# Kernel tuning notes

Hardware: AMD Instinct MI355X
Metric: run time of the kernel (lower is better)

The kernel has to match this reference:

```python
import jax, jax.numpy as jnp
import numpy as np

B, N, DIM = 8, 512, 768
H, DH = 12, 64
INNER = H * DH
MLP = 3072
DEPTH = 4
EPS = 1e-5
LS = 0.1  # LayerScale init_eps for depth <= 18


def _ln(x, scale):
    # flax LayerNorm(use_bias=False): (x-mean)/sqrt(var+eps) * scale
    mu = jnp.mean(x, axis=-1, keepdims=True)
    var = jnp.mean(jnp.square(x - mu), axis=-1, keepdims=True)
    return (x - mu) * jax.lax.rsqrt(var + EPS) * scale


def setup_inputs() -> dict:
    key = jax.random.key(0)
    ks = jax.random.split(key, 13)
    s = 0.02
    inp = {
        "x": jax.random.normal(ks[0], (B, N, DIM), jnp.float32),
        "ln1": jnp.ones((DEPTH, DIM), jnp.float32),
        "Wq": jax.random.normal(ks[1], (DEPTH, DIM, INNER), jnp.float32) * s,
        "Wkv": jax.random.normal(ks[2], (DEPTH, DIM, 2 * INNER), jnp.float32) * s,
        "mix_pre": jax.random.normal(ks[3], (DEPTH, H, H), jnp.float32) * 0.1,
        "mix_post": jax.random.normal(ks[4], (DEPTH, H, H), jnp.float32) * 0.1,
        "Wo": jax.random.normal(ks[5], (DEPTH, INNER, DIM), jnp.float32) * s,
        "bo": jnp.zeros((DEPTH, DIM), jnp.float32),
        "ln2": jnp.ones((DEPTH, DIM), jnp.float32),
        "W1": jax.random.normal(ks[6], (DEPTH, DIM, MLP), jnp.float32) * s,
        "b1": jnp.zeros((DEPTH, MLP), jnp.float32),
        "W2": jax.random.normal(ks[7], (DEPTH, MLP, DIM), jnp.float32) * s,
        "b2": jnp.zeros((DEPTH, DIM), jnp.float32),
    }
    return inp


def _block(x, p):
    ln1, Wq, Wkv, mp, mq, Wo, bo, ln2, W1, b1, W2, b2 = p
    scale = DH ** -0.5
    h = _ln(x, ln1)
    q = h @ Wq                                  # [b,n,inner]
    kv = h @ Wkv
    k, v = jnp.split(kv, 2, axis=-1)
    def to_heads(t):
        return t.reshape(B, N, H, DH).transpose(0, 2, 1, 3)  # b h n d
    q, k, v = to_heads(q), to_heads(k), to_heads(v)
    dots = jnp.einsum('bhid,bhjd->bhij', q, k) * scale
    dots = jnp.einsum('bhij,hg->bgij', dots, mp)   # talking-heads pre-softmax
    attn = jax.nn.softmax(dots, axis=-1)
    attn = jnp.einsum('bhij,hg->bgij', attn, mq)   # talking-heads post-softmax
    o = jnp.einsum('bhij,bhjd->bhid', attn, v)
    o = o.transpose(0, 2, 1, 3).reshape(B, N, INNER)
    x = (o @ Wo + bo) * LS + x
    h2 = _ln(x, ln2)
    x = ((jax.nn.gelu(h2 @ W1 + b1) @ W2) + b2) * LS + x
    return x, None


def reference(x, ln1, Wq, Wkv, mix_pre, mix_post, Wo, bo, ln2, W1, b1, W2, b2):
    params = (ln1, Wq, Wkv, mix_pre, mix_post, Wo, bo, ln2, W1, b1, W2, b2)
    out, _ = jax.lax.scan(_block, x, params)
    return out
```

## Files before the change

### kernel.cpp

```cpp
#include <hip/hip_runtime.h>


#define LSCALE 0.1f

typedef __bf16 bf16;
typedef __bf16 bf16x8 __attribute__((ext_vector_type(8)));
typedef __bf16 bf16x4 __attribute__((ext_vector_type(4)));
typedef unsigned short ushort4v __attribute__((ext_vector_type(4)));
typedef float  f32x4  __attribute__((ext_vector_type(4)));

__device__ __forceinline__ void g2l16(const void* g, void* l) {
    __builtin_amdgcn_global_load_lds(
        (const __attribute__((address_space(1))) void*)g,
        (__attribute__((address_space(3))) void*)l, 16, 0, 0);
}

template<int EPI, bool PLANA = false>
__global__ __launch_bounds__(256, 2)
void gemm_bt(const bf16* __restrict__ A, int lda, long saz1, long saz2,
             const bf16* __restrict__ Bt, int ldb, long sbz1, long sbz2,
             void* __restrict__ Cv, int ldc, long scz1, long scz2,
             int M, int N, int K, int zmod,
             const float* __restrict__ bias, float scale)
{
    __shared__ __align__(16) char smem[35840];
    bf16* As = (bf16*)smem;
    bf16* Bs = (bf16*)(smem + 16384);
    bf16* Cs = (bf16*)smem;

    const int z  = blockIdx.z;
    const int z1 = z / zmod, z2 = z - z1 * zmod;
    const bf16* Ab = A  + saz1 * (long)z1 + saz2 * (long)z2;
    const bf16* Bb = Bt + sbz1 * (long)z1 + sbz2 * (long)z2;

    const int m0 = blockIdx.x * 128, n0 = blockIdx.y * 128;
    const int tid = threadIdx.x, w = tid >> 6, l = tid & 63;
    const int wr = (w >> 1) * 64, wc = (w & 1) * 64;
    const int lr = l & 15, lq = l >> 4;
    const int srow = l >> 2, scol8 = (l & 3) * 8;

    long abase = 0;
    if constexpr (PLANA)
        abase = (long)(m0 >> 9) * 393216 + (long)((m0 & 511) + w * 32) * 64;

    f32x4 acc[4][4];
#pragma unroll
    for (int i = 0; i < 4; i++)
#pragma unroll
        for (int j = 0; j < 4; j++)
#pragma unroll
            for (int r = 0; r < 4; r++) acc[i][j][r] = 0.f;

    for (int k0 = 0; k0 < K; k0 += 64) {
        const bf16* Ag;
        int ldaa;
        if constexpr (PLANA) {
            Ag = Ab + abase + ((long)(k0 >> 6)) * 32768;
            ldaa = 64;
        } else {
            Ag = Ab + (long)(m0 + w * 32) * lda + k0;
            ldaa = lda;
        }
        const bf16* Bg = Bb + (long)(n0 + w * 32) * ldb + k0;
        g2l16(Ag + (long)srow * ldaa + scol8,             As + w * 1024);
        g2l16(Ag + (long)(srow + 16) * ldaa + scol8,      As + w * 1024 + 512);
        g2l16(Ag + (long)srow * ldaa + 32 + scol8,        As + 4096 + w * 1024);
        g2l16(Ag + (long)(srow + 16) * ldaa + 32 + scol8, As + 4096 + w * 1024 + 512);
        g2l16(Bg + (long)srow * ldb + scol8,             Bs + w * 1024);
        g2l16(Bg + (long)(srow + 16) * ldb + scol8,      Bs + w * 1024 + 512);
        g2l16(Bg + (long)srow * ldb + 32 + scol8,        Bs + 4096 + w * 1024);
        g2l16(Bg + (long)(srow + 16) * ldb + 32 + scol8, Bs + 4096 + w * 1024 + 512);
        __syncthreads();

#pragma unroll
        for (int hh = 0; hh < 2; hh++) {
            bf16x8 fa[4], fb[4];
#pragma unroll
            for (int i = 0; i < 4; i++)
                fa[i] = *(const bf16x8*)(As + hh * 4096 + (wr + i * 16 + lr) * 32 + lq * 8);
#pragma unroll
            for (int i = 0; i < 4; i++)
                fb[i] = *(const bf16x8*)(Bs + hh * 4096 + (wc + i * 16 + lr) * 32 + lq * 8);
#pragma unroll
            for (int mi = 0; mi < 4; mi++)
#pragma unroll
                for (int ni = 0; ni < 4; ni++)
                    acc[mi][ni] = __builtin_amdgcn_mfma_f32_16x16x32_bf16(
                        fa[mi], fb[ni], acc[mi][ni], 0, 0, 0);
        }
        __syncthreads();
    }

#pragma unroll
    for (int ni = 0; ni < 4; ni++) {
        const int col = wc + ni * 16 + lr;
        float bv = 0.f;
        if (EPI == 1) bv = bias[n0 + col];
#pragma unroll
        for (int mi = 0; mi < 4; mi++) {
#pragma unroll
            for (int r = 0; r < 4; r++) {
                const int row = wr + mi * 16 + lq * 4 + r;
                float v = acc[mi][ni][r];
                if (EPI == 0) {
                    v *= scale;
                } else if (EPI == 1) {
                    const float xx = v + bv;
                    const float u  = 0.7978845608f * (xx + 0.044715f * xx * xx * xx);
                    const float th = 1.f - 2.f / (__expf(2.f * u) + 1.f);
                    v = 0.5f * xx * (1.f + th);
                }
                Cs[row * 136 + col] = (bf16)v;
            }
        }
    }
    __syncthreads();

    const long cb = scz1 * (long)z1 + scz2 * (long)z2;
    const int rrow = tid >> 4, cg = tid & 15;
#pragma unroll
    for (int p = 0; p < 8; p++) {
        const int row = p * 16 + rrow;
        const bf16x8 v = *(const bf16x8*)(Cs + row * 136 + cg * 8);
        *(bf16x8*)((bf16*)Cv + cb + (long)(m0 + row) * ldc + n0 + cg * 8) = v;
    }
}

template<int PLANO>
__global__ __launch_bounds__(256, 4)
void gemm_av(const bf16* __restrict__ S, const bf16* __restrict__ qkvc,
             bf16* __restrict__ oc)
{
    __shared__ __align__(16) char av_smem[9728];
    bf16* As  = (bf16*)av_smem;
    bf16* Bst = (bf16*)(av_smem + 4096);
    bf16* Cs  = (bf16*)av_smem;

    const int z = blockIdx.y, b = z / 12, g = z - b * 12;
    const bf16* Ab;
    int sld;
    if constexpr (PLANO) {
        Ab = S + (long)b * 3145728 + g * 512;
        sld = 6144;
    } else {
        Ab = S + (long)z * 262144;
        sld = 512;
    }
    const bf16* Bb = qkvc + (long)b * 1179648 + 1536 + g * 64;

    const int i0 = blockIdx.x * 64;
    const int tid = threadIdx.x, w = tid >> 6, l = tid & 63;
    const int lr = l & 15, lq = l >> 4;
    const int srow = l >> 2, scol8 = (l & 3) * 8;
    const int kp = tid >> 4, dq = tid & 15;
    const int kcol = ((((kp >> 2) ^ ((dq >> 1) & 3)) << 3) | ((kp & 3) << 1));

    f32x4 acc[4];
#pragma unroll
    for (int j = 0; j < 4; j++)
#pragma unroll
        for (int r = 0; r < 4; r++) acc[j][r] = 0.f;

    unsigned short* Bw = (unsigned short*)Bst;

    for (int k0 = 0; k0 < 512; k0 += 32) {
        const bf16* Ag = Ab + (long)(i0 + w * 16) * sld + k0;
        g2l16(Ag + (long)srow * sld + scol8, As + w * 512);

        const bf16* Bg = Bb + (long)(k0 + 2 * kp) * 2304 + dq * 4;
        ushort4v u0 = *(const ushort4v*)(Bg);
        ushort4v u1 = *(const ushort4v*)(Bg + 2304);
#pragma unroll
        for (int r = 0; r < 4; r++) {
            unsigned p = (unsigned)u0[r] | ((unsigned)u1[r] << 16);
            *(unsigned*)(Bw + (dq * 4 + r) * 40 + kcol) = p;
        }
        __syncthreads();

        bf16x8 fa = *(const bf16x8*)(As + (w * 16 + lr) * 32 + lq * 8);
        bf16x8 fb[4];
#pragma unroll
        for (int i = 0; i < 4; i++) {
            const int d = i * 16 + lr;
            fb[i] = *(const bf16x8*)(Bst + d * 40 + ((lq ^ ((d >> 3) & 3)) << 3));
        }
#pragma unroll
        for (int ni = 0; ni < 4; ni++)
            acc[ni] = __builtin_amdgcn_mfma_f32_16x16x32_bf16(
                fa, fb[ni], acc[ni], 0, 0, 0);
        __syncthreads();
    }

    if constexpr (PLANO) {
#pragma unroll
        for (int ni = 0; ni < 4; ni++)
#pragma unroll
            for (int r = 0; r < 4; r++)
                Cs[(w * 16 + lq * 4 + r) * 68 + ni * 16 + lr] = (bf16)acc[ni][r];
        __syncthreads();
        const int rr = tid >> 2, c16 = (tid & 3) * 16;
        bf16* orow = oc + ((long)z * 512 + i0 + rr) * 64 + c16;
        *(bf16x8*)(orow)     = *(const bf16x8*)(Cs + rr * 68 + c16);
        *(bf16x8*)(orow + 8) = *(const bf16x8*)(Cs + rr * 68 + c16 + 8);
    } else {
        bf16* Cb = oc + (long)b * 1179648 + g * 64;
#pragma unroll
        for (int ni = 0; ni < 4; ni++) {
            const int gc = ni * 16 + lr;
#pragma unroll
            for (int r = 0; r < 4; r++) {
                const int gr = i0 + w * 16 + lq * 4 + r;
                Cb[(long)gr * 2304 + gc] = (bf16)acc[ni][r];
            }
        }
    }
}

__global__ __launch_bounds__(256)
void tconv_k(const float* __restrict__ in, bf16* __restrict__ out,
             int K, int N)
{
    __shared__ float t[32][33];
    const int n0 = blockIdx.x * 32, k0 = blockIdx.y * 32;
    const int x = threadIdx.x, y = threadIdx.y;
#pragma unroll
    for (int yy = 0; yy < 4; yy++)
        t[y + yy * 8][x] = in[(long)(k0 + y + yy * 8) * N + n0 + x];
    __syncthreads();
#pragma unroll
    for (int yy = 0; yy < 4; yy++)
        out[(long)(n0 + y + yy * 8) * K + k0 + x] = (bf16)t[x][y + yy * 8];
}

__global__ __launch_bounds__(256)
void pre_k(const float* __restrict__ Wq, const float* __restrict__ Wkv,
           const float* __restrict__ Wo, const float* __restrict__ W1,
           const float* __restrict__ W2, bf16* __restrict__ WtAll,
           const float* __restrict__ x, float* __restrict__ xf,
           const float* __restrict__ gam, bf16* __restrict__ hout)
{
    __shared__ __align__(16) char pmem[16640];
    const int bxg = blockIdx.x;
    const int t = threadIdx.x;
    if (bxg < 6912) {
        float (*st)[65] = (float(*)[65])pmem;
        const int L = bxg / 1728;
        int bx = bxg - L * 1728;
        bf16* WtL = WtAll + (long)L * 7077888;
        const float* src; bf16* dst; int K, N, ntn;
        if (bx < 144) {
            src = Wq + (long)L * 589824;   dst = WtL;            K = 768;  N = 768;  ntn = 12;
        } else if (bx < 432) {
            bx -= 144;
            src = Wkv + (long)L * 1179648; dst = WtL + 589824;   K = 768;  N = 1536; ntn = 24;
        } else if (bx < 576) {
            bx -= 432;
            src = Wo + (long)L * 589824;   dst = WtL + 1769472;  K = 768;  N = 768;  ntn = 12;
        } else if (bx < 1152) {
            bx -= 576;
            src = W1 + (long)L * 2359296;  dst = WtL + 2359296;  K = 768;  N = 3072; ntn = 48;
        } else {
            bx -= 1152;
            src = W2 + (long)L * 2359296;  dst = WtL + 4718592;  K = 3072; N = 768;  ntn = 12;
        }
        const int n0 = (bx % ntn) * 64, k0 = (bx / ntn) * 64;
        const int r = t >> 4, c4 = (t & 15) * 4;
#pragma unroll
        for (int rr = 0; rr < 4; rr++) {
            const f32x4 v = *(const f32x4*)(src + (long)(k0 + r + rr * 16) * N + n0 + c4);
            st[r + rr * 16][c4 + 0] = v[0];
            st[r + rr * 16][c4 + 1] = v[1];
            st[r + rr * 16][c4 + 2] = v[2];
            st[r + rr * 16][c4 + 3] = v[3];
        }
        __syncthreads();
        const int kc = (t & 7) * 8;
#pragma unroll
        for (int p = 0; p < 2; p++) {
            const int n = p * 32 + (t >> 3);
            bf16x8 o;
#pragma unroll
            for (int e = 0; e < 8; e++) o[e] = (bf16)st[kc + e][n];
            *(bf16x8*)(dst + (long)(n0 + n) * K + k0 + kc) = o;
        }
    } else {
        const int row = bxg - 6912;
        float* ps  = (float*)pmem;
        float* pss = (float*)pmem + 4;
        const float* xin = x + (long)row * 768;
        float* xr = xf + (long)row * 768;
        float v[3];
#pragma unroll
        for (int i = 0; i < 3; i++) {
            const int c = t + i * 256;
            const float xv = xin[c];
            xr[c] = xv;
            v[i] = xv;
        }
        float s  = v[0] + v[1] + v[2];
        float ss = v[0] * v[0] + v[1] * v[1] + v[2] * v[2];
#pragma unroll
        for (int off = 32; off; off >>= 1) {
            s  += __shfl_xor(s, off);
            ss += __shfl_xor(ss, off);
        }
        const int wv = t >> 6, l = t & 63;
        if (l == 0) { ps[wv] = s; pss[wv] = ss; }
        __syncthreads();
        s  = ps[0] + ps[1] + ps[2] + ps[3];
        ss = pss[0] + pss[1] + pss[2] + pss[3];
        const float mu = s * (1.f / 768.f);
        const float rs = rsqrtf(ss * (1.f / 768.f) - mu * mu + 1e-5f);
        bf16* orow = hout + (long)row * 768;
#pragma unroll
        for (int i = 0; i < 3; i++) {
            const int c = t + i * 256;
            orow[c] = (bf16)((v[i] - mu) * rs * gam[c]);
        }
    }
}

__global__ __launch_bounds__(256)
void lnres_k(float* __restrict__ xf, const bf16* __restrict__ P0,
             const bf16* __restrict__ P1, const float* __restrict__ bias,
             const float* __restrict__ gam, bf16* __restrict__ out,
             const float* __restrict__ src)
{
    const int row = blockIdx.x, t = threadIdx.x;
    float* xr = xf + (long)row * 768;
    float v[3];
#pragma unroll
    for (int i = 0; i < 3; i++) {
        const int c = t + i * 256;
        float xv;
        if (src) {
            xv = src[(long)row * 768 + c];
            xr[c] = xv;
        } else if (P0) {
            xv = xr[c] + LSCALE * ((float)P0[(long)row * 768 + c] +
                                   (float)P1[(long)row * 768 + c] + bias[c]);
            xr[c] = xv;
        } else {
            xv = xr[c];
        }
        v[i] = xv;
    }
    float s  = v[0] + v[1] + v[2];
    float ss = v[0] * v[0] + v[1] * v[1] + v[2] * v[2];
#pragma unroll
    for (int off = 32; off; off >>= 1) {
        s  += __shfl_xor(s, off);
        ss += __shfl_xor(ss, off);
    }
    __shared__ float ps[4], pss[4];
    const int wv = t >> 6, l = t & 63;
    if (l == 0) { ps[wv] = s; pss[wv] = ss; }
    __syncthreads();
    s  = ps[0] + ps[1] + ps[2] + ps[3];
    ss = pss[0] + pss[1] + pss[2] + pss[3];
    const float mu = s * (1.f / 768.f);
    const float rs = rsqrtf(ss * (1.f / 768.f) - mu * mu + 1e-5f);
    bf16* orow = out + (long)row * 768;
#pragma unroll
    for (int i = 0; i < 3; i++) {
        const int c = t + i * 256;
        orow[c] = (bf16)((v[i] - mu) * rs * gam[c]);
    }
}

__global__ __launch_bounds__(256)
void outres_k(const float* __restrict__ xf, const bf16* __restrict__ P0,
              const bf16* __restrict__ P1, const float* __restrict__ bias,
              float* __restrict__ out)
{
    const long i4 = ((long)blockIdx.x * 256 + threadIdx.x) * 4;
    const int c = (int)(i4 % 768);
    const f32x4 xv = *(const f32x4*)(xf + i4);
    const bf16x4 p0 = *(const bf16x4*)(P0 + i4);
    const bf16x4 p1 = *(const bf16x4*)(P1 + i4);
    const f32x4 bv = *(const f32x4*)(bias + c);
    f32x4 o;
#pragma unroll
    for (int e = 0; e < 4; e++)
        o[e] = xv[e] + LSCALE * ((float)p0[e] + (float)p1[e] + bv[e]);
    *(f32x4*)(out + i4) = o;
}

template<int CONTIG>
__global__ __launch_bounds__(256)
void mixsm_k(bf16* __restrict__ S, const float* __restrict__ mp,
             const float* __restrict__ mq)
{
    __shared__ float buf[12][512];
    __shared__ float rds[12];
    const int b = blockIdx.y, i = blockIdx.x, t = threadIdx.x;
    const long pstr = CONTIG ? 512 : 262144;
    bf16* Sb = CONTIG ? S + ((long)b * 512 + i) * 6144
                      : S + ((long)b * 12 * 512 + i) * 512;

    float s0[12], s1[12];
#pragma unroll
    for (int h = 0; h < 12; h++) {
        union { unsigned u; bf16 v[2]; } p;
        p.u = *(const unsigned*)(Sb + h * pstr + 2 * t);
        s0[h] = (float)p.v[0];
        s1[h] = (float)p.v[1];
    }
#pragma unroll
    for (int g = 0; g < 12; g++) {
        float a0 = 0.f, a1 = 0.f;
#pragma unroll
        for (int h = 0; h < 12; h++) {
            const float m = mp[h * 12 + g];
            a0 += s0[h] * m;
            a1 += s1[h] * m;
        }
        *(float2*)(&buf[g][2 * t]) = make_float2(a0, a1);
    }
    __syncthreads();

    const int wv = t >> 6, l = t & 63;
    for (int g = wv; g < 12; g += 4) {
        float mx = -3.0e38f;
#pragma unroll
        for (int k = 0; k < 8; k++) mx = fmaxf(mx, buf[g][l + 64 * k]);
#pragma unroll
        for (int off = 32; off; off >>= 1) mx = fmaxf(mx, __shfl_xor(mx, off));
        float sm = 0.f;
#pragma unroll
        for (int k = 0; k < 8; k++) {
            const float e = __expf(buf[g][l + 64 * k] - mx);
            buf[g][l + 64 * k] = e;
            sm += e;
        }
#pragma unroll
        for (int off = 32; off; off >>= 1) sm += __shfl_xor(sm, off);
        if (l == 0) rds[g] = 1.f / sm;
    }
    __syncthreads();

    float e0[12], e1[12];
#pragma unroll
    for (int h = 0; h < 12; h++) {
        const float2 ee = *(const float2*)(&buf[h][2 * t]);
        const float rd = rds[h];
        e0[h] = ee.x * rd;
        e1[h] = ee.y * rd;
    }
#pragma unroll
    for (int g = 0; g < 12; g++) {
        float a0 = 0.f, a1 = 0.f;
#pragma unroll
        for (int h = 0; h < 12; h++) {
            const float m = mq[h * 12 + g];
            a0 += e0[h] * m;
            a1 += e1[h] * m;
        }
        union { unsigned u; bf16 v[2]; } p;
        p.v[0] = (bf16)a0;
        p.v[1] = (bf16)a1;
        *(unsigned*)(Sb + g * pstr + 2 * t) = p.u;
    }
}

extern "C" void kernel_launch(void* const* d_in, const int* in_sizes, int n_in,
                              void* d_out, int out_size, void* d_ws, size_t ws_size,
                              hipStream_t stream)
{
    (void)in_sizes; (void)n_in; (void)out_size;
    const float* x   = (const float*)d_in[0];
    const float* ln1 = (const float*)d_in[1];
    const float* Wq  = (const float*)d_in[2];
    const float* Wkv = (const float*)d_in[3];
    const float* mp  = (const float*)d_in[4];
    const float* mq  = (const float*)d_in[5];
    const float* Wo  = (const float*)d_in[6];
    const float* bo  = (const float*)d_in[7];
    const float* ln2 = (const float*)d_in[8];
    const float* W1  = (const float*)d_in[9];
    const float* b1  = (const float*)d_in[10];
    const float* W2  = (const float*)d_in[11];
    const float* b2  = (const float*)d_in[12];

    char* ws = (char*)d_ws;
    float* xf  = (float*)(ws);
    bf16* h    = (bf16*)(ws + 12582912);
    bf16* qkv  = (bf16*)(ws + 18874368);
    bf16* S    = (bf16*)(ws + 37748736);
    bf16* mid  = S;
    bf16* P0   = h;
    bf16* P1w2 = qkv;
    bf16* P1wo = S;
    const long P1W2_OFF = 3145728;
    const long P1WO_OFF = 12582912;

    const dim3 tb(32, 8);

    if (ws_size >= 150994944ull) {
        bf16* WtAll = (bf16*)(ws + 88080384);
        bf16* oP    = (bf16*)(ws + 144703488);

        pre_k<<<11008, 256, 0, stream>>>(Wq, Wkv, Wo, W1, W2, WtAll,
                                         x, xf, ln1, h);

        for (int L = 0; L < 4; L++) {
            bf16* WtL = WtAll + (long)L * 7077888;

            if (L > 0)
                lnres_k<<<4096, 256, 0, stream>>>(xf, P0, P1w2, b2 + (L - 1) * 768,
                                                  ln1 + L * 768, h, nullptr);

            gemm_bt<0><<<dim3(32, 18, 1), 256, 0, stream>>>(
                h, 768, 0, 0, WtL, 768, 0, 0,
                qkv, 2304, 0, 0, 4096, 2304, 768, 1, nullptr, 1.f);

            gemm_bt<0><<<dim3(4, 4, 96), 256, 0, stream>>>(
                qkv,       2304, 1179648, 64,
                qkv + 768, 2304, 1179648, 64,
                S,         6144, 3145728, 512,
                512, 512, 64, 12, nullptr, 0.125f);

            mixsm_k<1><<<dim3(512, 8), 256, 0, stream>>>(S, mp + L * 144, mq + L * 144);

            gemm_av<1><<<dim3(8, 96), 256, 0, stream>>>(S, qkv, oP);

            gemm_bt<4, true><<<dim3(32, 6, 2), 256, 0, stream>>>(
                oP, 64, 0, 196608, WtL + 1769472, 768, 0, 384,
                P0, 768, 0, P1WO_OFF, 4096, 768, 384, 2, nullptr, 1.f);

            lnres_k<<<4096, 256, 0, stream>>>(xf, P0, P1wo, bo + L * 768,
                                              ln2 + L * 768, h, nullptr);

            gemm_bt<1><<<dim3(32, 24, 1), 256, 0, stream>>>(
                h, 768, 0, 0, WtL + 2359296, 768, 0, 0,
                mid, 3072, 0, 0, 4096, 3072, 768, 1, b1 + L * 3072, 1.f);

            gemm_bt<4><<<dim3(32, 6, 2), 256, 0, stream>>>(
                mid, 3072, 0, 1536, WtL + 4718592, 3072, 0, 1536,
                P0, 768, 0, P1W2_OFF, 4096, 768, 1536, 2, nullptr, 1.f);
        }
    } else {
        bf16* Wt = (bf16*)(ws + 62914560);

        for (int L = 0; L < 4; L++) {
            tconv_k<<<dim3(24, 24), tb, 0, stream>>>(Wq + (long)L * 589824, Wt, 768, 768);
            tconv_k<<<dim3(48, 24), tb, 0, stream>>>(Wkv + (long)L * 1179648, Wt + 589824, 768, 1536);

            if (L == 0)
                lnres_k<<<4096, 256, 0, stream>>>(xf, nullptr, nullptr, nullptr,
                                                  ln1 + L * 768, h, x);
            else
                lnres_k<<<4096, 256, 0, stream>>>(xf, P0, P1w2, b2 + (L - 1) * 768,
                                                  ln1 + L * 768, h, nullptr);

            gemm_bt<0><<<dim3(32, 18, 1), 256, 0, stream>>>(
                h, 768, 0, 0, Wt, 768, 0, 0,
                qkv, 2304, 0, 0, 4096, 2304, 768, 1, nullptr, 1.f);

            for (int c = 0; c < 2; c++) {
                const long qb = (long)c * 4718592;
                gemm_bt<0><<<dim3(4, 4, 48), 256, 0, stream>>>(
                    qkv + qb,       2304, 1179648, 64,
                    qkv + 768 + qb, 2304, 1179648, 64,
                    S,               512, 3145728, 262144,
                    512, 512, 64, 12, nullptr, 0.125f);

                mixsm_k<0><<<dim3(512, 4), 256, 0, stream>>>(S, mp + L * 144, mq + L * 144);

                gemm_av<0><<<dim3(8, 48), 256, 0, stream>>>(S, qkv + qb, qkv + qb);
            }

            tconv_k<<<dim3(24, 24), tb, 0, stream>>>(Wo + (long)L * 589824, Wt, 768, 768);
            gemm_bt<4><<<dim3(32, 6, 2), 256, 0, stream>>>(
                qkv, 2304, 0, 384, Wt, 768, 0, 384,
                P0, 768, 0, P1WO_OFF, 4096, 768, 384, 2, nullptr, 1.f);

            lnres_k<<<4096, 256, 0, stream>>>(xf, P0, P1wo, bo + L * 768,
                                              ln2 + L * 768, h, nullptr);

            tconv_k<<<dim3(96, 24), tb, 0, stream>>>(W1 + (long)L * 2359296, Wt, 768, 3072);
            gemm_bt<1><<<dim3(32, 24, 1), 256, 0, stream>>>(
                h, 768, 0, 0, Wt, 768, 0, 0,
                mid, 3072, 0, 0, 4096, 3072, 768, 1, b1 + L * 3072, 1.f);

            tconv_k<<<dim3(24, 96), tb, 0, stream>>>(W2 + (long)L * 2359296, Wt, 3072, 768);
            gemm_bt<4><<<dim3(32, 6, 2), 256, 0, stream>>>(
                mid, 3072, 0, 1536, Wt, 3072, 0, 1536,
                P0, 768, 0, P1W2_OFF, 4096, 768, 1536, 2, nullptr, 1.f);
        }
    }

    outres_k<<<3072, 256, 0, stream>>>(xf, P0, P1w2, b2 + 3 * 768, (float*)d_out);
}
```

Before: 872.3 us.

## Spread weight transpose-convert tiles into trailing blocks of layer-0/1 GEMMs

The upfront pre-kernel now converts only the layer-0 Q/KV weights. The remaining fp32-to-bf16 transpose tiles are appended as extra blocks to several early GEMM launches (layer 0 QKV, FFN1, FFN2 and layer 1 FFN1). Each conversion is placed before the GEMM that first consumes it, and those extra blocks can fill idle CUs during GEMM tails instead of forming a serialized prologue. Correctness depends on the tile-index ranges lining up with where each converted weight is first used. The added blocks may also contend for bandwidth with the GEMM blocks.

```diff
diff --git a/kernel.cpp b/kernel.cpp
--- a/kernel.cpp
+++ b/kernel.cpp
@@ -15,25 +15,92 @@
         (__attribute__((address_space(3))) void*)l, 16, 0, 0);
 }
 
-template<int EPI, bool PLANA = false>
+__device__ __forceinline__ void tconv_tile(int T, int t,
+    const float* __restrict__ Wq, const float* __restrict__ Wkv,
+    const float* __restrict__ Wo, const float* __restrict__ W1,
+    const float* __restrict__ W2, bf16* __restrict__ WtAll, char* pmem)
+{
+    float (*st)[65] = (float(*)[65])pmem;
+    const int L = T / 1728;
+    int bx = T - L * 1728;
+    bf16* WtL = WtAll + (long)L * 7077888;
+    const float* src; bf16* dst; int K, N, ntn;
+    if (bx < 144) {
+        src = Wq + (long)L * 589824;   dst = WtL;            K = 768;  N = 768;  ntn = 12;
+    } else if (bx < 432) {
+        bx -= 144;
+        src = Wkv + (long)L * 1179648; dst = WtL + 589824;   K = 768;  N = 1536; ntn = 24;
+    } else if (bx < 576) {
+        bx -= 432;
+        src = Wo + (long)L * 589824;   dst = WtL + 1769472;  K = 768;  N = 768;  ntn = 12;
+    } else if (bx < 1152) {
+        bx -= 576;
+        src = W1 + (long)L * 2359296;  dst = WtL + 2359296;  K = 768;  N = 3072; ntn = 48;
+    } else {
+        bx -= 1152;
+        src = W2 + (long)L * 2359296;  dst = WtL + 4718592;  K = 3072; N = 768;  ntn = 12;
+    }
+    const int n0 = (bx % ntn) * 64, k0 = (bx / ntn) * 64;
+    const int r = t >> 4, c4 = (t & 15) * 4;
+#pragma unroll
+    for (int rr = 0; rr < 4; rr++) {
+        const f32x4 v = *(const f32x4*)(src + (long)(k0 + r + rr * 16) * N + n0 + c4);
+        st[r + rr * 16][c4 + 0] = v[0];
+        st[r + rr * 16][c4 + 1] = v[1];
+        st[r + rr * 16][c4 + 2] = v[2];
+        st[r + rr * 16][c4 + 3] = v[3];
+    }
+    __syncthreads();
+    const int kc = (t & 7) * 8;
+#pragma unroll
+    for (int p = 0; p < 2; p++) {
+        const int n = p * 32 + (t >> 3);
+        bf16x8 o;
+#pragma unroll
+        for (int e = 0; e < 8; e++) o[e] = (bf16)st[kc + e][n];
+        *(bf16x8*)(dst + (long)(n0 + n) * K + k0 + kc) = o;
+    }
+}
+
+template<int EPI, bool PLANA = false, bool RID = false>
 __global__ __launch_bounds__(256, 2)
 void gemm_bt(const bf16* __restrict__ A, int lda, long saz1, long saz2,
              const bf16* __restrict__ Bt, int ldb, long sbz1, long sbz2,
              void* __restrict__ Cv, int ldc, long scz1, long scz2,
              int M, int N, int K, int zmod,
-             const float* __restrict__ bias, float scale)
+             const float* __restrict__ bias, float scale,
+             int mt, int nt, int rbase,
+             const float* __restrict__ tWq, const float* __restrict__ tWkv,
+             const float* __restrict__ tWo, const float* __restrict__ tW1,
+             const float* __restrict__ tW2, bf16* __restrict__ tWt)
 {
     __shared__ __align__(16) char smem[35840];
     bf16* As = (bf16*)smem;
     bf16* Bs = (bf16*)(smem + 16384);
     bf16* Cs = (bf16*)smem;
 
-    const int z  = blockIdx.z;
+    int bm, bn, z;
+    if constexpr (RID) {
+        const int nbg = mt * nt * zmod;
+        const int bx = blockIdx.x;
+        if (bx >= nbg) {
+            tconv_tile(rbase + bx - nbg, threadIdx.x,
+                       tWq, tWkv, tWo, tW1, tW2, tWt, smem);
+            return;
+        }
+        bm = bx % mt;
+        const int r = bx / mt;
+        bn = r % nt;
+        z  = r / nt;
+    } else {
+        bm = blockIdx.x; bn = blockIdx.y; z = blockIdx.z;
+    }
+
     const int z1 = z / zmod, z2 = z - z1 * zmod;
     const bf16* Ab = A  + saz1 * (long)z1 + saz2 * (long)z2;
     const bf16* Bb = Bt + sbz1 * (long)z1 + sbz2 * (long)z2;
 
-    const int m0 = blockIdx.x * 128, n0 = blockIdx.y * 128;
+    const int m0 = bm * 128, n0 = bn * 128;
     const int tid = threadIdx.x, w = tid >> 6, l = tid & 63;
     const int wr = (w >> 1) * 64, wc = (w & 1) * 64;
     const int lr = l & 15, lq = l >> 4;
@@ -233,58 +300,19 @@
 }
 
 __global__ __launch_bounds__(256)
-void pre_k(const float* __restrict__ Wq, const float* __restrict__ Wkv,
-           const float* __restrict__ Wo, const float* __restrict__ W1,
-           const float* __restrict__ W2, bf16* __restrict__ WtAll,
-           const float* __restrict__ x, float* __restrict__ xf,
-           const float* __restrict__ gam, bf16* __restrict__ hout)
+void pre2_k(const float* __restrict__ Wq, const float* __restrict__ Wkv,
+            const float* __restrict__ Wo, const float* __restrict__ W1,
+            const float* __restrict__ W2, bf16* __restrict__ WtAll,
+            const float* __restrict__ x, float* __restrict__ xf,
+            const float* __restrict__ gam, bf16* __restrict__ hout)
 {
     __shared__ __align__(16) char pmem[16640];
     const int bxg = blockIdx.x;
     const int t = threadIdx.x;
-    if (bxg < 6912) {
-        float (*st)[65] = (float(*)[65])pmem;
-        const int L = bxg / 1728;
-        int bx = bxg - L * 1728;
-        bf16* WtL = WtAll + (long)L * 7077888;
-        const float* src; bf16* dst; int K, N, ntn;
-        if (bx < 144) {
-            src = Wq + (long)L * 589824;   dst = WtL;            K = 768;  N = 768;  ntn = 12;
-        } else if (bx < 432) {
-            bx -= 144;
-            src = Wkv + (long)L * 1179648; dst = WtL + 589824;   K = 768;  N = 1536; ntn = 24;
-        } else if (bx < 576) {
-            bx -= 432;
-            src = Wo + (long)L * 589824;   dst = WtL + 1769472;  K = 768;  N = 768;  ntn = 12;
-        } else if (bx < 1152) {
-            bx -= 576;
-            src = W1 + (long)L * 2359296;  dst = WtL + 2359296;  K = 768;  N = 3072; ntn = 48;
-        } else {
-            bx -= 1152;
-            src = W2 + (long)L * 2359296;  dst = WtL + 4718592;  K = 3072; N = 768;  ntn = 12;
-        }
-        const int n0 = (bx % ntn) * 64, k0 = (bx / ntn) * 64;
-        const int r = t >> 4, c4 = (t & 15) * 4;
-#pragma unroll
-        for (int rr = 0; rr < 4; rr++) {
-            const f32x4 v = *(const f32x4*)(src + (long)(k0 + r + rr * 16) * N + n0 + c4);
-            st[r + rr * 16][c4 + 0] = v[0];
-            st[r + rr * 16][c4 + 1] = v[1];
-            st[r + rr * 16][c4 + 2] = v[2];
-            st[r + rr * 16][c4 + 3] = v[3];
-        }
-        __syncthreads();
-        const int kc = (t & 7) * 8;
-#pragma unroll
-        for (int p = 0; p < 2; p++) {
-            const int n = p * 32 + (t >> 3);
-            bf16x8 o;
-#pragma unroll
-            for (int e = 0; e < 8; e++) o[e] = (bf16)st[kc + e][n];
-            *(bf16x8*)(dst + (long)(n0 + n) * K + k0 + kc) = o;
-        }
+    if (bxg < 432) {
+        tconv_tile(bxg, t, Wq, Wkv, Wo, W1, W2, WtAll, pmem);
     } else {
-        const int row = bxg - 6912;
+        const int row = bxg - 432;
         float* ps  = (float*)pmem;
         float* pss = (float*)pmem + 4;
         const float* xin = x + (long)row * 768;
@@ -500,7 +528,7 @@
         bf16* WtAll = (bf16*)(ws + 88080384);
         bf16* oP    = (bf16*)(ws + 144703488);
 
-        pre_k<<<11008, 256, 0, stream>>>(Wq, Wkv, Wo, W1, W2, WtAll,
+        pre2_k<<<4528, 256, 0, stream>>>(Wq, Wkv, Wo, W1, W2, WtAll,
                                          x, xf, ln1, h);
 
         for (int L = 0; L < 4; L++) {
@@ -510,15 +538,23 @@
                 lnres_k<<<4096, 256, 0, stream>>>(xf, P0, P1w2, b2 + (L - 1) * 768,
                                                   ln1 + L * 768, h, nullptr);
 
-            gemm_bt<0><<<dim3(32, 18, 1), 256, 0, stream>>>(
-                h, 768, 0, 0, WtL, 768, 0, 0,
-                qkv, 2304, 0, 0, 4096, 2304, 768, 1, nullptr, 1.f);
+            if (L == 0)
+                gemm_bt<0, false, true><<<576 + 1728, 256, 0, stream>>>(
+                    h, 768, 0, 0, WtL, 768, 0, 0,
+                    qkv, 2304, 0, 0, 4096, 2304, 768, 1, nullptr, 1.f,
+                    32, 18, 432, Wq, Wkv, Wo, W1, W2, WtAll);
+            else
+                gemm_bt<0><<<dim3(32, 18, 1), 256, 0, stream>>>(
+                    h, 768, 0, 0, WtL, 768, 0, 0,
+                    qkv, 2304, 0, 0, 4096, 2304, 768, 1, nullptr, 1.f,
+                    0, 0, 0, nullptr, nullptr, nullptr, nullptr, nullptr, nullptr);
 
             gemm_bt<0><<<dim3(4, 4, 96), 256, 0, stream>>>(
                 qkv,       2304, 1179648, 64,
                 qkv + 768, 2304, 1179648, 64,
                 S,         6144, 3145728, 512,
-                512, 512, 64, 12, nullptr, 0.125f);
+                512, 512, 64, 12, nullptr, 0.125f,
+                0, 0, 0, nullptr, nullptr, nullptr, nullptr, nullptr, nullptr);
 
             mixsm_k<1><<<dim3(512, 8), 256, 0, stream>>>(S, mp + L * 144, mq + L * 144);
 
@@ -526,18 +562,38 @@
 
             gemm_bt<4, true><<<dim3(32, 6, 2), 256, 0, stream>>>(
                 oP, 64, 0, 196608, WtL + 1769472, 768, 0, 384,
-                P0, 768, 0, P1WO_OFF, 4096, 768, 384, 2, nullptr, 1.f);
+                P0, 768, 0, P1WO_OFF, 4096, 768, 384, 2, nullptr, 1.f,
+                0, 0, 0, nullptr, nullptr, nullptr, nullptr, nullptr, nullptr);
 
             lnres_k<<<4096, 256, 0, stream>>>(xf, P0, P1wo, bo + L * 768,
                                               ln2 + L * 768, h, nullptr);
 
-            gemm_bt<1><<<dim3(32, 24, 1), 256, 0, stream>>>(
-                h, 768, 0, 0, WtL + 2359296, 768, 0, 0,
-                mid, 3072, 0, 0, 4096, 3072, 768, 1, b1 + L * 3072, 1.f);
-
-            gemm_bt<4><<<dim3(32, 6, 2), 256, 0, stream>>>(
-                mid, 3072, 0, 1536, WtL + 4718592, 3072, 0, 1536,
-                P0, 768, 0, P1W2_OFF, 4096, 768, 1536, 2, nullptr, 1.f);
+            if (L == 0)
+                gemm_bt<1, false, true><<<768 + 1728, 256, 0, stream>>>(
+                    h, 768, 0, 0, WtL + 2359296, 768, 0, 0,
+                    mid, 3072, 0, 0, 4096, 3072, 768, 1, b1 + L * 3072, 1.f,
+                    32, 24, 2160, Wq, Wkv, Wo, W1, W2, WtAll);
+            else if (L == 1)
+                gemm_bt<1, false, true><<<768 + 1296, 256, 0, stream>>>(
+                    h, 768, 0, 0, WtL + 2359296, 768, 0, 0,
+                    mid, 3072, 0, 0, 4096, 3072, 768, 1, b1 + L * 3072, 1.f,
+                    32, 24, 5616, Wq, Wkv, Wo, W1, W2, WtAll);
+            else
+                gemm_bt<1><<<dim3(32, 24, 1), 256, 0, stream>>>(
+                    h, 768, 0, 0, WtL + 2359296, 768, 0, 0,
+                    mid, 3072, 0, 0, 4096, 3072, 768, 1, b1 + L * 3072, 1.f,
+                    0, 0, 0, nullptr, nullptr, nullptr, nullptr, nullptr, nullptr);
+
+            if (L == 0)
+                gemm_bt<4, false, true><<<384 + 1728, 256, 0, stream>>>(
+                    mid, 3072, 0, 1536, WtL + 4718592, 3072, 0, 1536,
+                    P0, 768, 0, P1W2_OFF, 4096, 768, 1536, 2, nullptr, 1.f,
+                    32, 6, 3888, Wq, Wkv, Wo, W1, W2, WtAll);
+            else
+                gemm_bt<4><<<dim3(32, 6, 2), 256, 0, stream>>>(
+                    mid, 3072, 0, 1536, WtL + 4718592, 3072, 0, 1536,
+                    P0, 768, 0, P1W2_OFF, 4096, 768, 1536, 2, nullptr, 1.f,
+                    0, 0, 0, nullptr, nullptr, nullptr, nullptr, nullptr, nullptr);
         }
     } else {
         bf16* Wt = (bf16*)(ws + 62914560);
@@ -555,7 +611,8 @@
 
             gemm_bt<0><<<dim3(32, 18, 1), 256, 0, stream>>>(
                 h, 768, 0, 0, Wt, 768, 0, 0,
-                qkv, 2304, 0, 0, 4096, 2304, 768, 1, nullptr, 1.f);
+                qkv, 2304, 0, 0, 4096, 2304, 768, 1, nullptr, 1.f,
+                0, 0, 0, nullptr, nullptr, nullptr, nullptr, nullptr, nullptr);
 
             for (int c = 0; c < 2; c++) {
                 const long qb = (long)c * 4718592;
@@ -563,7 +620,8 @@
                     qkv + qb,       2304, 1179648, 64,
                     qkv + 768 + qb, 2304, 1179648, 64,
                     S,               512, 3145728, 262144,
-                    512, 512, 64, 12, nullptr, 0.125f);
+                    512, 512, 64, 12, nullptr, 0.125f,
+                    0, 0, 0, nullptr, nullptr, nullptr, nullptr, nullptr, nullptr);
 
                 mixsm_k<0><<<dim3(512, 4), 256, 0, stream>>>(S, mp + L * 144, mq + L * 144);
 
@@ -573,7 +631,8 @@
             tconv_k<<<dim3(24, 24), tb, 0, stream>>>(Wo + (long)L * 589824, Wt, 768, 768);
             gemm_bt<4><<<dim3(32, 6, 2), 256, 0, stream>>>(
                 qkv, 2304, 0, 384, Wt, 768, 0, 384,
-                P0, 768, 0, P1WO_OFF, 4096, 768, 384, 2, nullptr, 1.f);
+                P0, 768, 0, P1WO_OFF, 4096, 768, 384, 2, nullptr, 1.f,
+                0, 0, 0, nullptr, nullptr, nullptr, nullptr, nullptr, nullptr);
 
             lnres_k<<<4096, 256, 0, stream>>>(xf, P0, P1wo, bo + L * 768,
                                               ln2 + L * 768, h, nullptr);
@@ -581,12 +640,14 @@
             tconv_k<<<dim3(96, 24), tb, 0, stream>>>(W1 + (long)L * 2359296, Wt, 768, 3072);
             gemm_bt<1><<<dim3(32, 24, 1), 256, 0, stream>>>(
                 h, 768, 0, 0, Wt, 768, 0, 0,
-                mid, 3072, 0, 0, 4096, 3072, 768, 1, b1 + L * 3072, 1.f);
+                mid, 3072, 0, 0, 4096, 3072, 768, 1, b1 + L * 3072, 1.f,
+                0, 0, 0, nullptr, nullptr, nullptr, nullptr, nullptr, nullptr);
 
             tconv_k<<<dim3(24, 96), tb, 0, stream>>>(W2 + (long)L * 2359296, Wt, 3072, 768);
             gemm_bt<4><<<dim3(32, 6, 2), 256, 0, stream>>>(
                 mid, 3072, 0, 1536, Wt, 3072, 0, 1536,
-                P0, 768, 0, P1W2_OFF, 4096, 768, 1536, 2, nullptr, 1.f);
+                P0, 768, 0, P1W2_OFF, 4096, 768, 1536, 2, nullptr, 1.f,
+                0, 0, 0, nullptr, nullptr, nullptr, nullptr, nullptr, nullptr);
         }
     }
 
```

Result: no change. 858.6 us (-1.6%).
